# Kernel tuning notes

Hardware: AMD Instinct MI355X
Metric: run time of the kernel (lower is better)

Reference implementation:

```python
import jax, jax.numpy as jnp
import numpy as np

N, D_IN, D_OUT, K = 8192, 64, 128, 16


def setup_inputs() -> dict:
    key = jax.random.key(0)
    k1, k2, k3 = jax.random.split(key, 3)
    x = jax.random.normal(k1, (N, D_IN), dtype=jnp.float32)
    W1 = jax.random.normal(k2, (2 * D_IN, D_OUT), dtype=jnp.float32) * 0.05
    b1 = jnp.zeros((D_OUT,), dtype=jnp.float32)
    W2 = jax.random.normal(k3, (D_OUT, D_OUT), dtype=jnp.float32) * 0.05
    b2 = jnp.zeros((D_OUT,), dtype=jnp.float32)
    return {"x": x, "W1": W1, "b1": b1, "W2": W2, "b2": b2, "k": K}


def reference(x, W1, b1, W2, b2, k):
    # dynamic kNN graph (PyG knn(x, x, k) includes self as nearest neighbor)
    sq = jnp.sum(x * x, axis=-1)                      # [N]
    dist = sq[:, None] + sq[None, :] - 2.0 * (x @ x.T)  # [N, N] squared dists
    _, idx = jax.lax.top_k(-dist, k)                  # [N, k] nearest indices
    x_j = x[idx]                                      # [N, k, D_IN] gather
    x_i = jnp.broadcast_to(x[:, None, :], x_j.shape)  # [N, k, D_IN]
    e = jnp.concatenate([x_i, x_j - x_i], axis=-1)    # [N, k, 2*D_IN]
    h = jax.nn.relu(e @ W1 + b1) @ W2 + b2            # [N, k, D_OUT]
    return jnp.mean(h, axis=1)                        # mean aggregation -> [N, D_OUT]
```

## Files before the change

### kernel.cpp

```cpp
#include <hip/hip_runtime.h>

#define N 8192
#define DIN 64
#define DOUT 128
#define KNN 16
#define MSAMP 2048
#define NBX 8
#define CAND_R 64
#define CAND_C (NBX * CAND_R)
#define EPS 1.0f
#define DELTA_Q 64
#define VCAP 128
#define ROWS_PRE 16

typedef unsigned long long u64;
typedef __attribute__((ext_vector_type(8))) short bf16x8;
typedef __attribute__((ext_vector_type(4))) float floatx4;

__device__ __forceinline__ unsigned mono(float f) {
    unsigned u = __float_as_uint(f);
    return (u & 0x80000000u) ? ~u : (u | 0x80000000u);
}
__device__ __forceinline__ unsigned short f2bf(float f) {
    unsigned u = __float_as_uint(f);
    return (unsigned short)((u + 0x7FFFu + ((u >> 16) & 1u)) >> 16);
}
__device__ __forceinline__ unsigned qdist(float dist) {
    int q = (int)(dist * 128.0f) + 2;
    q = max(q, 0); return (unsigned)min(q, 65535);
}

__global__ __launch_bounds__(256) void k_pre(const float* __restrict__ x,
                                             const float* __restrict__ W1,
                                             const float* __restrict__ b1,
                                             float* __restrict__ sq,
                                             float* __restrict__ sqs,
                                             unsigned short* __restrict__ Xh,
                                             float* __restrict__ U,
                                             float* __restrict__ V) {
    __shared__ float xs[ROWS_PRE][DIN];
    int t = threadIdx.x;
    int r0 = blockIdx.x * ROWS_PRE;
    float4 xv = ((const float4*)x)[(size_t)r0 * (DIN / 4) + t];
    ((float4*)xs)[t] = xv;
    ushort4 h4;
    h4.x = f2bf(xv.x); h4.y = f2bf(xv.y);
    h4.z = f2bf(xv.z); h4.w = f2bf(xv.w);
    *(ushort4*)&Xh[r0 * DIN + t * 4] = h4;
    __syncthreads();
    if (t < ROWS_PRE) {
        const float4* xr = (const float4*)xs[t];
        float s0 = 0.f, s1 = 0.f, s2 = 0.f, s3 = 0.f;
#pragma unroll
        for (int q = 0; q < DIN / 4; ++q) {
            float4 a = xr[q];
            s0 = fmaf(a.x, a.x, s0); s1 = fmaf(a.y, a.y, s1);
            s2 = fmaf(a.z, a.z, s2); s3 = fmaf(a.w, a.w, s3);
        }
        float sv = (s0 + s1) + (s2 + s3);
        sq[r0 + t] = sv;
        if ((t & 3) == 0) sqs[(r0 + t) >> 2] = sv;
    }
    int o = t & 127, g = t >> 7;
    float aU[8], aV[8];
#pragma unroll
    for (int u = 0; u < 8; ++u) { aU[u] = 0.f; aV[u] = 0.f; }
    for (int kk = 0; kk < DIN; ++kk) {
        float whi = W1[kk * DOUT + o];
        float wlo = W1[(DIN + kk) * DOUT + o];
        float wd = whi - wlo;
#pragma unroll
        for (int u = 0; u < 8; ++u) {
            float xvv = xs[g * 8 + u][kk];
            aU[u] = fmaf(xvv, wd, aU[u]);
            aV[u] = fmaf(xvv, wlo, aV[u]);
        }
    }
    float bb = b1[o];
#pragma unroll
    for (int u = 0; u < 8; ++u) {
        int r = r0 + g * 8 + u;
        U[(size_t)r * DOUT + o] = aU[u] + bb;
        V[(size_t)r * DOUT + o] = aV[u];
    }
}

__global__ __launch_bounds__(512, 4) void k_pretau(const unsigned short* __restrict__ Xh,
                                                   const float* __restrict__ sq,
                                                   const float* __restrict__ sqs,
                                                   float* __restrict__ tauf) {
    __shared__ __align__(16) unsigned short qls[16 * MSAMP];
    int tid = threadIdx.x, w = tid >> 6, l = tid & 63;
    int m = l & 15, quad = l >> 4, ko = quad * 8;
    int rt = blockIdx.x;
    int irow = rt * 16 + m;
    size_t arow = (size_t)irow * DIN;
    bf16x8 iH0 = *(const bf16x8*)(Xh + arow + ko);
    bf16x8 iH1 = *(const bf16x8*)(Xh + arow + 32 + ko);
    float si = sq[irow];
    int swz = (m & 7) << 4;
    for (int it = 0; it < 16; ++it) {
        int s16 = w * 256 + it * 16;
        size_t srowA = (size_t)(4 * (s16 + m)) * DIN;
        bf16x8 sH0 = *(const bf16x8*)(Xh + srowA + ko);
        bf16x8 sH1 = *(const bf16x8*)(Xh + srowA + 32 + ko);
        floatx4 acc = {0.f, 0.f, 0.f, 0.f};
        acc = __builtin_amdgcn_mfma_f32_16x16x32_bf16(sH0, iH0, acc, 0, 0, 0);
        acc = __builtin_amdgcn_mfma_f32_16x16x32_bf16(sH1, iH1, acc, 0, 0, 0);
        int sc0 = s16 + quad * 4;
        float4 sj = *(const float4*)(sqs + sc0);
        unsigned q0 = qdist(fmaf(-2.0f, acc[0], si + sj.x));
        unsigned q1 = qdist(fmaf(-2.0f, acc[1], si + sj.y));
        unsigned q2 = qdist(fmaf(-2.0f, acc[2], si + sj.z));
        unsigned q3 = qdist(fmaf(-2.0f, acc[3], si + sj.w));
        u64 pk = (u64)q0 | ((u64)q1 << 16) | ((u64)q2 << 32) | ((u64)q3 << 48);
        *(u64*)&qls[m * MSAMP + (sc0 ^ swz)] = pk;
    }
    __syncthreads();
#pragma unroll
    for (int rr = 0; rr < 2; ++rr) {
        int rsub = w * 2 + rr;
        unsigned v[MSAMP / 64];
#pragma unroll
        for (int u = 0; u < MSAMP / 64; ++u)
            v[u] = qls[rsub * MSAMP + l + 64 * u];
        unsigned p = 0;
#pragma unroll
        for (int b = 15; b >= 0; --b) {
            unsigned c16 = p | (1u << b);
            int cnt = 0;
#pragma unroll
            for (int u = 0; u < MSAMP / 64; ++u)
                cnt += __popcll(__ballot(v[u] < c16));
            if (cnt < 16) p = c16;
        }
        if (l == 0) tauf[rt * 16 + rsub] = (float)p * (1.0f / 128.0f);
    }
}

__global__ __launch_bounds__(256, 4) void k_main(const unsigned short* __restrict__ Xh,
                                                 const float* __restrict__ sq,
                                                 const float* __restrict__ tauf,
                                                 unsigned* __restrict__ cand,
                                                 unsigned* __restrict__ cntpart) {
    __shared__ __align__(16) short ldsH[64 * 72];
    int tid = threadIdx.x, w = tid >> 6, l = tid & 63;
    int m = l & 15, ko = (l >> 4) * 8;
    int bx = blockIdx.x;
    int rt = blockIdx.y * 4 + w;
    size_t arow = (size_t)(rt * 16 + m) * DIN;
    bf16x8 aH0 = *(const bf16x8*)(Xh + arow + ko);
    bf16x8 aH1 = *(const bf16x8*)(Xh + arow + 32 + ko);
    int rg[4]; float T[4]; float si[4]; int rowcnt[4];
#pragma unroll
    for (int reg = 0; reg < 4; ++reg) {
        rg[reg] = rt * 16 + (l >> 4) * 4 + reg;
        si[reg] = sq[rg[reg]];
        T[reg] = tauf[rg[reg]] + EPS - si[reg];
        rowcnt[reg] = 0;
    }
    int qs = l & 48;
    unsigned lmask = (1u << (l & 15)) - 1u;
    int srw = tid >> 3, scol8 = (tid & 7) * 8;

    for (int st = 0; st < 16; ++st) {
        int jbase = bx * 1024 + st * 64;
        __syncthreads();
        *(bf16x8*)&ldsH[srw * 72 + scol8] =
            *(const bf16x8*)(Xh + (size_t)(jbase + srw) * DIN + scol8);
        *(bf16x8*)&ldsH[(srw + 32) * 72 + scol8] =
            *(const bf16x8*)(Xh + (size_t)(jbase + srw + 32) * DIN + scol8);
        __syncthreads();
#pragma unroll
        for (int it = 0; it < 4; ++it) {
            int br = it * 16 + m;
            bf16x8 bH0 = *(const bf16x8*)&ldsH[br * 72 + ko];
            bf16x8 bH1 = *(const bf16x8*)&ldsH[br * 72 + 32 + ko];
            floatx4 acc = {0.f, 0.f, 0.f, 0.f};
            acc = __builtin_amdgcn_mfma_f32_16x16x32_bf16(aH0, bH0, acc, 0, 0, 0);
            acc = __builtin_amdgcn_mfma_f32_16x16x32_bf16(aH1, bH1, acc, 0, 0, 0);
            int jcol = jbase + it * 16 + m;
            float sqj = sq[jcol];
#pragma unroll
            for (int reg = 0; reg < 4; ++reg) {
                float tv = fmaf(-2.0f, acc[reg], sqj);
                bool pass = tv <= T[reg];
                u64 bal = __ballot(pass);
                if (bal) {
                    unsigned m16 = (unsigned)((bal >> qs) & 0xFFFFull);
                    if (pass) {
                        int slot = rowcnt[reg] + __popc(m16 & lmask);
                        if (slot < CAND_R)
                            cand[(size_t)rg[reg] * CAND_C + bx * CAND_R + slot] =
                                (qdist(tv + si[reg]) << 16) | (unsigned)jcol;
                    }
                    rowcnt[reg] += __popc(m16);
                }
            }
        }
    }
    if ((l & 15) == 0) {
#pragma unroll
        for (int reg = 0; reg < 4; ++reg)
            cntpart[rg[reg] * NBX + bx] = (unsigned)min(rowcnt[reg], CAND_R);
    }
}

__global__ __launch_bounds__(256) void k_exact(const float* __restrict__ x,
                                               const float* __restrict__ sq,
                                               const unsigned* __restrict__ cntpart,
                                               const unsigned* __restrict__ cand,
                                               int* __restrict__ knn) {
    __shared__ unsigned cj[4][CAND_C];
    __shared__ unsigned short vlist[4][VCAP];
    __shared__ u64 ekeys[4][VCAP];
    int w = threadIdx.x >> 6, l = threadIdx.x & 63;
    int row = blockIdx.x * 4 + w;
    int base = 0;
#pragma unroll
    for (int b = 0; b < NBX; ++b) {
        int c = (int)cntpart[row * NBX + b];
        c = min(c, CAND_R);
        if (l < c) cj[w][base + l] = cand[(size_t)row * CAND_C + b * CAND_R + l];
        base += c;
    }
    __syncthreads();
    unsigned kk[CAND_C / 64], qq[CAND_C / 64];
#pragma unroll
    for (int u = 0; u < CAND_C / 64; ++u) {
        int idx = l + 64 * u;
        kk[u] = (idx < base) ? cj[w][idx] : 0xFFFFFFFFu;
        qq[u] = (idx < base) ? (kk[u] >> 16) : 0xFFFFFFFFu;
    }
    unsigned p = 0;
#pragma unroll
    for (int b = 15; b >= 0; --b) {
        unsigned c16 = p | (1u << b);
        int cnt = 0;
#pragma unroll
        for (int u = 0; u < CAND_C / 64; ++u)
            cnt += __popcll(__ballot(qq[u] < c16));
        if (cnt < 16) p = c16;
    }
    unsigned thr = p + DELTA_Q;
    int nv = 0;
    u64 lm = (l == 63) ? 0xFFFFFFFFFFFFFFFFull >> 1 : (1ull << l) - 1ull;
#pragma unroll
    for (int u = 0; u < CAND_C / 64; ++u) {
        bool pred = qq[u] <= thr;
        u64 bal = __ballot(pred);
        int slot = nv + __popcll(bal & lm);
        if (pred && slot < VCAP) vlist[w][slot] = (unsigned short)(kk[u] & 0xFFFFu);
        nv += __popcll(bal);
    }
    nv = min(nv, VCAP);
    __syncthreads();
    float sqi = sq[row];
    const float* xi = x + (size_t)row * DIN;
#pragma unroll
    for (int r = 0; r < VCAP / 64; ++r) {
        int v = l + 64 * r;
        if (v < nv) {
            int j = (int)vlist[w][v];
            const float4* bj = (const float4*)(x + (size_t)j * DIN);
            float4 rb[16];
#pragma unroll
            for (int q = 0; q < DIN / 4; ++q) rb[q] = bj[q];
            float s0 = 0.f, s1 = 0.f, s2 = 0.f, s3 = 0.f;
#pragma unroll
            for (int q = 0; q < DIN / 4; ++q) {
                s0 = fmaf(xi[4 * q + 0], rb[q].x, s0);
                s1 = fmaf(xi[4 * q + 1], rb[q].y, s1);
                s2 = fmaf(xi[4 * q + 2], rb[q].z, s2);
                s3 = fmaf(xi[4 * q + 3], rb[q].w, s3);
            }
            float d = (s0 + s1) + (s2 + s3);
            float dist = fmaf(-2.0f, d, sqi + sq[j]);
            ekeys[w][v] = ((u64)mono(dist) << 32) | (unsigned)j;
        }
    }
#pragma unroll
    for (int r = 0; r < VCAP / 64; ++r) {
        int v = l + 64 * r;
        if (v < nv) {
            u64 mykey = ekeys[w][v];
            int rank = 0;
            for (int i = 0; i < nv; ++i)
                rank += (ekeys[w][i] < mykey) ? 1 : 0;
            if (rank < KNN)
                knn[row * KNN + rank] = (int)(unsigned)(mykey & 0xFFFFFFFFull);
        }
    }
}

__global__ __launch_bounds__(256) void k_aggout(const float* __restrict__ U,
                                                const float* __restrict__ V,
                                                const int* __restrict__ knn,
                                                const float* __restrict__ W2,
                                                const float* __restrict__ b2,
                                                float* __restrict__ out) {
    __shared__ float ag[8][DOUT];
    __shared__ float w2t[32 * DOUT];
    int t = threadIdx.x;
    int o = t & 127, g = t >> 7;
    int i0 = blockIdx.x * 8 + g * 4;
#pragma unroll
    for (int r = 0; r < 4; ++r) {
        int i = i0 + r;
        float u = U[(size_t)i * DOUT + o];
        const int* nb = knn + i * KNN;
        float acc = 0.f;
#pragma unroll
        for (int q = 0; q < KNN; ++q)
            acc += fmaxf(u + V[(size_t)nb[q] * DOUT + o], 0.0f);
        ag[g * 4 + r][o] = acc * (1.0f / KNN);
    }
    float a2[4] = {0.f, 0.f, 0.f, 0.f};
#pragma unroll
    for (int tile = 0; tile < 4; ++tile) {
        __syncthreads();
#pragma unroll
        for (int u = 0; u < 4; ++u)
            ((float4*)w2t)[t + u * 256] =
                ((const float4*)(W2 + tile * 32 * DOUT))[t + u * 256];
        __syncthreads();
#pragma unroll 8
        for (int kk = 0; kk < 32; ++kk) {
            float wv = w2t[kk * DOUT + o];
#pragma unroll
            for (int r = 0; r < 4; ++r)
                a2[r] = fmaf(ag[g * 4 + r][tile * 32 + kk], wv, a2[r]);
        }
    }
    float bb = b2[o];
#pragma unroll
    for (int r = 0; r < 4; ++r)
        out[(size_t)(i0 + r) * DOUT + o] = a2[r] + bb;
}

extern "C" void kernel_launch(void* const* d_in, const int* in_sizes, int n_in,
                              void* d_out, int out_size, void* d_ws, size_t ws_size,
                              hipStream_t stream) {
    const float* x  = (const float*)d_in[0];
    const float* W1 = (const float*)d_in[1];
    const float* b1 = (const float*)d_in[2];
    const float* W2 = (const float*)d_in[3];
    const float* b2 = (const float*)d_in[4];
    float* out = (float*)d_out;

    char* ws = (char*)d_ws;
    float*          sq      = (float*)(ws);
    float*          sqs     = (float*)(ws + 32768);
    float*          tauf    = (float*)(ws + 40960);
    int*            knn     = (int*)(ws + 73728);
    unsigned short* Xh      = (unsigned short*)(ws + 655360);
    unsigned*       cntpart = (unsigned*)(ws + 1703936);
    float*          U       = (float*)(ws + 2097152);
    float*          V       = (float*)(ws + 6291456);
    unsigned*       cand    = (unsigned*)(ws + 10485760);

    k_pre<<<N / ROWS_PRE, 256, 0, stream>>>(x, W1, b1, sq, sqs, Xh, U, V);
    k_pretau<<<N / 16, 512, 0, stream>>>(Xh, sq, sqs, tauf);
    k_main<<<dim3(NBX, 128), 256, 0, stream>>>(Xh, sq, tauf, cand, cntpart);
    k_exact<<<N / 4, 256, 0, stream>>>(x, sq, cntpart, cand, knn);
    k_aggout<<<N / 8, 256, 0, stream>>>(U, V, knn, W2, b2, out);
}
```

Before: 182.0 us.

## Fuse pre, tau and candidate scan into one persistent kernel with grid barriers

Merges the preprocessing, threshold-estimation and candidate-scan kernels into a single 512-block persistent kernel that separates the phases with atomic grid barriers. It also merges exact kNN selection with aggregation and output, so the kNN indices stay in LDS instead of round-tripping through global memory. The aim is to cut kernel launch gaps and the tail effects between stages. In exchange it relies on all 512 blocks being co-resident for the spin barrier, and it changes the per-block work split (512 threads, one row-load per stage in the scan).

New measurement: 240.6 us. 32.2% more time.

```diff
diff --git a/kernel.cpp b/kernel.cpp
--- a/kernel.cpp
+++ b/kernel.cpp
@@ -11,7 +11,7 @@
 #define EPS 1.0f
 #define DELTA_Q 64
 #define VCAP 128
-#define ROWS_PRE 16
+#define NBLK 512
 
 typedef unsigned long long u64;
 typedef __attribute__((ext_vector_type(8))) short bf16x8;
@@ -30,312 +30,325 @@
     q = max(q, 0); return (unsigned)min(q, 65535);
 }
 
-__global__ __launch_bounds__(256) void k_pre(const float* __restrict__ x,
-                                             const float* __restrict__ W1,
-                                             const float* __restrict__ b1,
-                                             float* __restrict__ sq,
-                                             float* __restrict__ sqs,
-                                             unsigned short* __restrict__ Xh,
-                                             float* __restrict__ U,
-                                             float* __restrict__ V) {
-    __shared__ float xs[ROWS_PRE][DIN];
+__device__ __forceinline__ void gridbar(unsigned* cnt) {
+    __syncthreads();
+    if (threadIdx.x == 0) {
+        __hip_atomic_fetch_add(cnt, 1u, __ATOMIC_RELEASE, __HIP_MEMORY_SCOPE_AGENT);
+        while (__hip_atomic_load(cnt, __ATOMIC_RELAXED, __HIP_MEMORY_SCOPE_AGENT)
+               < (unsigned)NBLK)
+            __builtin_amdgcn_s_sleep(16);
+        __threadfence();
+    }
+    __syncthreads();
+}
+
+__global__ __launch_bounds__(512, 4) void k_scan(
+    const float* __restrict__ x, const float* __restrict__ W1,
+    const float* __restrict__ b1, float* __restrict__ sq,
+    float* __restrict__ sqs, unsigned short* __restrict__ Xh,
+    float* __restrict__ U, float* __restrict__ V,
+    float* __restrict__ tauf, unsigned* __restrict__ cand,
+    unsigned* __restrict__ cntpart, unsigned* __restrict__ bar)
+{
+    __shared__ __align__(16) unsigned char smem[65536];
     int t = threadIdx.x;
-    int r0 = blockIdx.x * ROWS_PRE;
-    float4 xv = ((const float4*)x)[(size_t)r0 * (DIN / 4) + t];
-    ((float4*)xs)[t] = xv;
-    ushort4 h4;
-    h4.x = f2bf(xv.x); h4.y = f2bf(xv.y);
-    h4.z = f2bf(xv.z); h4.w = f2bf(xv.w);
-    *(ushort4*)&Xh[r0 * DIN + t * 4] = h4;
-    __syncthreads();
-    if (t < ROWS_PRE) {
-        const float4* xr = (const float4*)xs[t];
-        float s0 = 0.f, s1 = 0.f, s2 = 0.f, s3 = 0.f;
-#pragma unroll
-        for (int q = 0; q < DIN / 4; ++q) {
-            float4 a = xr[q];
-            s0 = fmaf(a.x, a.x, s0); s1 = fmaf(a.y, a.y, s1);
-            s2 = fmaf(a.z, a.z, s2); s3 = fmaf(a.w, a.w, s3);
-        }
-        float sv = (s0 + s1) + (s2 + s3);
-        sq[r0 + t] = sv;
-        if ((t & 3) == 0) sqs[(r0 + t) >> 2] = sv;
-    }
-    int o = t & 127, g = t >> 7;
-    float aU[8], aV[8];
-#pragma unroll
-    for (int u = 0; u < 8; ++u) { aU[u] = 0.f; aV[u] = 0.f; }
-    for (int kk = 0; kk < DIN; ++kk) {
-        float whi = W1[kk * DOUT + o];
-        float wlo = W1[(DIN + kk) * DOUT + o];
-        float wd = whi - wlo;
-#pragma unroll
-        for (int u = 0; u < 8; ++u) {
-            float xvv = xs[g * 8 + u][kk];
-            aU[u] = fmaf(xvv, wd, aU[u]);
-            aV[u] = fmaf(xvv, wlo, aV[u]);
-        }
-    }
-    float bb = b1[o];
-#pragma unroll
-    for (int u = 0; u < 8; ++u) {
-        int r = r0 + g * 8 + u;
-        U[(size_t)r * DOUT + o] = aU[u] + bb;
-        V[(size_t)r * DOUT + o] = aV[u];
-    }
-}
-
-__global__ __launch_bounds__(512, 4) void k_pretau(const unsigned short* __restrict__ Xh,
-                                                   const float* __restrict__ sq,
-                                                   const float* __restrict__ sqs,
-                                                   float* __restrict__ tauf) {
-    __shared__ __align__(16) unsigned short qls[16 * MSAMP];
-    int tid = threadIdx.x, w = tid >> 6, l = tid & 63;
-    int m = l & 15, quad = l >> 4, ko = quad * 8;
-    int rt = blockIdx.x;
-    int irow = rt * 16 + m;
-    size_t arow = (size_t)irow * DIN;
-    bf16x8 iH0 = *(const bf16x8*)(Xh + arow + ko);
-    bf16x8 iH1 = *(const bf16x8*)(Xh + arow + 32 + ko);
-    float si = sq[irow];
-    int swz = (m & 7) << 4;
-    for (int it = 0; it < 16; ++it) {
-        int s16 = w * 256 + it * 16;
-        size_t srowA = (size_t)(4 * (s16 + m)) * DIN;
-        bf16x8 sH0 = *(const bf16x8*)(Xh + srowA + ko);
-        bf16x8 sH1 = *(const bf16x8*)(Xh + srowA + 32 + ko);
-        floatx4 acc = {0.f, 0.f, 0.f, 0.f};
-        acc = __builtin_amdgcn_mfma_f32_16x16x32_bf16(sH0, iH0, acc, 0, 0, 0);
-        acc = __builtin_amdgcn_mfma_f32_16x16x32_bf16(sH1, iH1, acc, 0, 0, 0);
-        int sc0 = s16 + quad * 4;
-        float4 sj = *(const float4*)(sqs + sc0);
-        unsigned q0 = qdist(fmaf(-2.0f, acc[0], si + sj.x));
-        unsigned q1 = qdist(fmaf(-2.0f, acc[1], si + sj.y));
-        unsigned q2 = qdist(fmaf(-2.0f, acc[2], si + sj.z));
-        unsigned q3 = qdist(fmaf(-2.0f, acc[3], si + sj.w));
-        u64 pk = (u64)q0 | ((u64)q1 << 16) | ((u64)q2 << 32) | ((u64)q3 << 48);
-        *(u64*)&qls[m * MSAMP + (sc0 ^ swz)] = pk;
-    }
-    __syncthreads();
-#pragma unroll
-    for (int rr = 0; rr < 2; ++rr) {
-        int rsub = w * 2 + rr;
-        unsigned v[MSAMP / 64];
-#pragma unroll
-        for (int u = 0; u < MSAMP / 64; ++u)
-            v[u] = qls[rsub * MSAMP + l + 64 * u];
+    int b = blockIdx.x;
+
+    {
+        float (*xs)[DIN] = (float (*)[DIN])smem;
+        int r0 = b * 16;
+        if (t < 256) {
+            float4 xv = ((const float4*)x)[(size_t)r0 * (DIN / 4) + t];
+            ((float4*)xs)[t] = xv;
+            ushort4 h4;
+            h4.x = f2bf(xv.x); h4.y = f2bf(xv.y);
+            h4.z = f2bf(xv.z); h4.w = f2bf(xv.w);
+            *(ushort4*)&Xh[r0 * DIN + t * 4] = h4;
+        }
+        __syncthreads();
+        if (t < 16) {
+            const float4* xr = (const float4*)xs[t];
+            float s0 = 0.f, s1 = 0.f, s2 = 0.f, s3 = 0.f;
+#pragma unroll
+            for (int q = 0; q < DIN / 4; ++q) {
+                float4 a = xr[q];
+                s0 = fmaf(a.x, a.x, s0); s1 = fmaf(a.y, a.y, s1);
+                s2 = fmaf(a.z, a.z, s2); s3 = fmaf(a.w, a.w, s3);
+            }
+            float sv = (s0 + s1) + (s2 + s3);
+            sq[r0 + t] = sv;
+            if ((t & 3) == 0) sqs[(r0 + t) >> 2] = sv;
+        }
+        int o = t & 127, g = t >> 7;
+        float aU[4], aV[4];
+#pragma unroll
+        for (int u = 0; u < 4; ++u) { aU[u] = 0.f; aV[u] = 0.f; }
+        for (int kk = 0; kk < DIN; ++kk) {
+            float whi = W1[kk * DOUT + o];
+            float wlo = W1[(DIN + kk) * DOUT + o];
+            float wd = whi - wlo;
+#pragma unroll
+            for (int u = 0; u < 4; ++u) {
+                float xvv = xs[g * 4 + u][kk];
+                aU[u] = fmaf(xvv, wd, aU[u]);
+                aV[u] = fmaf(xvv, wlo, aV[u]);
+            }
+        }
+        float bb = b1[o];
+#pragma unroll
+        for (int u = 0; u < 4; ++u) {
+            int r = r0 + g * 4 + u;
+            U[(size_t)r * DOUT + o] = aU[u] + bb;
+            V[(size_t)r * DOUT + o] = aV[u];
+        }
+    }
+    gridbar(bar);
+    {
+        unsigned short* qls = (unsigned short*)smem;
+        int w = t >> 6, l = t & 63;
+        int m = l & 15, quad = l >> 4, ko = quad * 8;
+        int irow = b * 16 + m;
+        size_t arow = (size_t)irow * DIN;
+        bf16x8 iH0 = *(const bf16x8*)(Xh + arow + ko);
+        bf16x8 iH1 = *(const bf16x8*)(Xh + arow + 32 + ko);
+        float si = sq[irow];
+        int swz = (m & 7) << 4;
+        for (int it = 0; it < 16; ++it) {
+            int s16 = w * 256 + it * 16;
+            size_t srowA = (size_t)(4 * (s16 + m)) * DIN;
+            bf16x8 sH0 = *(const bf16x8*)(Xh + srowA + ko);
+            bf16x8 sH1 = *(const bf16x8*)(Xh + srowA + 32 + ko);
+            floatx4 acc = {0.f, 0.f, 0.f, 0.f};
+            acc = __builtin_amdgcn_mfma_f32_16x16x32_bf16(sH0, iH0, acc, 0, 0, 0);
+            acc = __builtin_amdgcn_mfma_f32_16x16x32_bf16(sH1, iH1, acc, 0, 0, 0);
+            int sc0 = s16 + quad * 4;
+            float4 sj = *(const float4*)(sqs + sc0);
+            unsigned q0 = qdist(fmaf(-2.0f, acc[0], si + sj.x));
+            unsigned q1 = qdist(fmaf(-2.0f, acc[1], si + sj.y));
+            unsigned q2 = qdist(fmaf(-2.0f, acc[2], si + sj.z));
+            unsigned q3 = qdist(fmaf(-2.0f, acc[3], si + sj.w));
+            u64 pk = (u64)q0 | ((u64)q1 << 16) | ((u64)q2 << 32) | ((u64)q3 << 48);
+            *(u64*)&qls[m * MSAMP + (sc0 ^ swz)] = pk;
+        }
+        __syncthreads();
+#pragma unroll
+        for (int rr = 0; rr < 2; ++rr) {
+            int rsub = w * 2 + rr;
+            unsigned v[MSAMP / 64];
+#pragma unroll
+            for (int u = 0; u < MSAMP / 64; ++u)
+                v[u] = qls[rsub * MSAMP + l + 64 * u];
+            unsigned p = 0;
+#pragma unroll
+            for (int bb = 15; bb >= 0; --bb) {
+                unsigned c16 = p | (1u << bb);
+                int cnt = 0;
+#pragma unroll
+                for (int u = 0; u < MSAMP / 64; ++u)
+                    cnt += __popcll(__ballot(v[u] < c16));
+                if (cnt < 16) p = c16;
+            }
+            if (l == 0) tauf[b * 16 + rsub] = (float)p * (1.0f / 128.0f);
+        }
+    }
+    gridbar(bar + 1);
+    {
+        short* ldsH = (short*)smem;
+        int w = t >> 6, l = t & 63;
+        int m = l & 15, ko = (l >> 4) * 8;
+        int bx = b & 7;
+        int rt = (b >> 3) * 8 + w;
+        size_t arow = (size_t)(rt * 16 + m) * DIN;
+        bf16x8 aH0 = *(const bf16x8*)(Xh + arow + ko);
+        bf16x8 aH1 = *(const bf16x8*)(Xh + arow + 32 + ko);
+        int rg[4]; float T[4]; float si[4]; int rowcnt[4];
+#pragma unroll
+        for (int reg = 0; reg < 4; ++reg) {
+            rg[reg] = rt * 16 + (l >> 4) * 4 + reg;
+            si[reg] = sq[rg[reg]];
+            T[reg] = tauf[rg[reg]] + EPS - si[reg];
+            rowcnt[reg] = 0;
+        }
+        int qs = l & 48;
+        unsigned lmask = (1u << (l & 15)) - 1u;
+        int srw = t >> 3, scol8 = (t & 7) * 8;
+
+        for (int st = 0; st < 16; ++st) {
+            int jbase = bx * 1024 + st * 64;
+            __syncthreads();
+            *(bf16x8*)&ldsH[srw * 72 + scol8] =
+                *(const bf16x8*)(Xh + (size_t)(jbase + srw) * DIN + scol8);
+            __syncthreads();
+#pragma unroll
+            for (int it = 0; it < 4; ++it) {
+                int br = it * 16 + m;
+                bf16x8 bH0 = *(const bf16x8*)&ldsH[br * 72 + ko];
+                bf16x8 bH1 = *(const bf16x8*)&ldsH[br * 72 + 32 + ko];
+                floatx4 acc = {0.f, 0.f, 0.f, 0.f};
+                acc = __builtin_amdgcn_mfma_f32_16x16x32_bf16(aH0, bH0, acc, 0, 0, 0);
+                acc = __builtin_amdgcn_mfma_f32_16x16x32_bf16(aH1, bH1, acc, 0, 0, 0);
+                int jcol = jbase + it * 16 + m;
+                float sqj = sq[jcol];
+#pragma unroll
+                for (int reg = 0; reg < 4; ++reg) {
+                    float tv = fmaf(-2.0f, acc[reg], sqj);
+                    bool pass = tv <= T[reg];
+                    u64 bal = __ballot(pass);
+                    if (bal) {
+                        unsigned m16 = (unsigned)((bal >> qs) & 0xFFFFull);
+                        if (pass) {
+                            int slot = rowcnt[reg] + __popc(m16 & lmask);
+                            if (slot < CAND_R)
+                                cand[(size_t)rg[reg] * CAND_C + bx * CAND_R + slot] =
+                                    (qdist(tv + si[reg]) << 16) | (unsigned)jcol;
+                        }
+                        rowcnt[reg] += __popc(m16);
+                    }
+                }
+            }
+        }
+        if ((l & 15) == 0) {
+#pragma unroll
+            for (int reg = 0; reg < 4; ++reg)
+                cntpart[rg[reg] * NBX + bx] = (unsigned)min(rowcnt[reg], CAND_R);
+        }
+    }
+}
+
+__global__ __launch_bounds__(256) void k_post(
+    const float* __restrict__ x, const float* __restrict__ sq,
+    const unsigned* __restrict__ cntpart, const unsigned* __restrict__ cand,
+    const float* __restrict__ U, const float* __restrict__ V,
+    const float* __restrict__ W2, const float* __restrict__ b2,
+    float* __restrict__ out)
+{
+    __shared__ union {
+        struct { unsigned cj[4][CAND_C];
+                 unsigned short vlist[4][VCAP];
+                 u64 ekeys[4][VCAP]; } e;
+        struct { float ag[4][DOUT];
+                 float w2t[32 * DOUT]; } a;
+    } sm;
+    __shared__ int knn_s[4][KNN];
+    int t = threadIdx.x;
+    int w = t >> 6, l = t & 63;
+    int row = blockIdx.x * 4 + w;
+    {
+        int base = 0;
+#pragma unroll
+        for (int b = 0; b < NBX; ++b) {
+            int c = (int)cntpart[row * NBX + b];
+            c = min(c, CAND_R);
+            if (l < c) sm.e.cj[w][base + l] =
+                cand[(size_t)row * CAND_C + b * CAND_R + l];
+            base += c;
+        }
+        __syncthreads();
+        unsigned kk[CAND_C / 64], qq[CAND_C / 64];
+#pragma unroll
+        for (int u = 0; u < CAND_C / 64; ++u) {
+            int idx = l + 64 * u;
+            kk[u] = (idx < base) ? sm.e.cj[w][idx] : 0xFFFFFFFFu;
+            qq[u] = (idx < base) ? (kk[u] >> 16) : 0xFFFFFFFFu;
+        }
         unsigned p = 0;
 #pragma unroll
         for (int b = 15; b >= 0; --b) {
             unsigned c16 = p | (1u << b);
             int cnt = 0;
 #pragma unroll
-            for (int u = 0; u < MSAMP / 64; ++u)
-                cnt += __popcll(__ballot(v[u] < c16));
+            for (int u = 0; u < CAND_C / 64; ++u)
+                cnt += __popcll(__ballot(qq[u] < c16));
             if (cnt < 16) p = c16;
         }
-        if (l == 0) tauf[rt * 16 + rsub] = (float)p * (1.0f / 128.0f);
-    }
-}
-
-__global__ __launch_bounds__(256, 4) void k_main(const unsigned short* __restrict__ Xh,
-                                                 const float* __restrict__ sq,
-                                                 const float* __restrict__ tauf,
-                                                 unsigned* __restrict__ cand,
-                                                 unsigned* __restrict__ cntpart) {
-    __shared__ __align__(16) short ldsH[64 * 72];
-    int tid = threadIdx.x, w = tid >> 6, l = tid & 63;
-    int m = l & 15, ko = (l >> 4) * 8;
-    int bx = blockIdx.x;
-    int rt = blockIdx.y * 4 + w;
-    size_t arow = (size_t)(rt * 16 + m) * DIN;
-    bf16x8 aH0 = *(const bf16x8*)(Xh + arow + ko);
-    bf16x8 aH1 = *(const bf16x8*)(Xh + arow + 32 + ko);
-    int rg[4]; float T[4]; float si[4]; int rowcnt[4];
-#pragma unroll
-    for (int reg = 0; reg < 4; ++reg) {
-        rg[reg] = rt * 16 + (l >> 4) * 4 + reg;
-        si[reg] = sq[rg[reg]];
-        T[reg] = tauf[rg[reg]] + EPS - si[reg];
-        rowcnt[reg] = 0;
-    }
-    int qs = l & 48;
-    unsigned lmask = (1u << (l & 15)) - 1u;
-    int srw = tid >> 3, scol8 = (tid & 7) * 8;
-
-    for (int st = 0; st < 16; ++st) {
-        int jbase = bx * 1024 + st * 64;
+        unsigned thr = p + DELTA_Q;
+        int nv = 0;
+        u64 lm = (l == 63) ? 0xFFFFFFFFFFFFFFFFull >> 1 : (1ull << l) - 1ull;
+#pragma unroll
+        for (int u = 0; u < CAND_C / 64; ++u) {
+            bool pred = qq[u] <= thr;
+            u64 bal = __ballot(pred);
+            int slot = nv + __popcll(bal & lm);
+            if (pred && slot < VCAP)
+                sm.e.vlist[w][slot] = (unsigned short)(kk[u] & 0xFFFFu);
+            nv += __popcll(bal);
+        }
+        nv = min(nv, VCAP);
         __syncthreads();
-        *(bf16x8*)&ldsH[srw * 72 + scol8] =
-            *(const bf16x8*)(Xh + (size_t)(jbase + srw) * DIN + scol8);
-        *(bf16x8*)&ldsH[(srw + 32) * 72 + scol8] =
-            *(const bf16x8*)(Xh + (size_t)(jbase + srw + 32) * DIN + scol8);
-        __syncthreads();
-#pragma unroll
-        for (int it = 0; it < 4; ++it) {
-            int br = it * 16 + m;
-            bf16x8 bH0 = *(const bf16x8*)&ldsH[br * 72 + ko];
-            bf16x8 bH1 = *(const bf16x8*)&ldsH[br * 72 + 32 + ko];
-            floatx4 acc = {0.f, 0.f, 0.f, 0.f};
-            acc = __builtin_amdgcn_mfma_f32_16x16x32_bf16(aH0, bH0, acc, 0, 0, 0);
-            acc = __builtin_amdgcn_mfma_f32_16x16x32_bf16(aH1, bH1, acc, 0, 0, 0);
-            int jcol = jbase + it * 16 + m;
-            float sqj = sq[jcol];
-#pragma unroll
-            for (int reg = 0; reg < 4; ++reg) {
-                float tv = fmaf(-2.0f, acc[reg], sqj);
-                bool pass = tv <= T[reg];
-                u64 bal = __ballot(pass);
-                if (bal) {
-                    unsigned m16 = (unsigned)((bal >> qs) & 0xFFFFull);
-                    if (pass) {
-                        int slot = rowcnt[reg] + __popc(m16 & lmask);
-                        if (slot < CAND_R)
-                            cand[(size_t)rg[reg] * CAND_C + bx * CAND_R + slot] =
-                                (qdist(tv + si[reg]) << 16) | (unsigned)jcol;
-                    }
-                    rowcnt[reg] += __popc(m16);
+        float sqi = sq[row];
+        const float* xi = x + (size_t)row * DIN;
+#pragma unroll
+        for (int r = 0; r < VCAP / 64; ++r) {
+            int v = l + 64 * r;
+            if (v < nv) {
+                int j = (int)sm.e.vlist[w][v];
+                const float4* bj = (const float4*)(x + (size_t)j * DIN);
+                float4 rb[16];
+#pragma unroll
+                for (int q = 0; q < DIN / 4; ++q) rb[q] = bj[q];
+                float s0 = 0.f, s1 = 0.f, s2 = 0.f, s3 = 0.f;
+#pragma unroll
+                for (int q = 0; q < DIN / 4; ++q) {
+                    s0 = fmaf(xi[4 * q + 0], rb[q].x, s0);
+                    s1 = fmaf(xi[4 * q + 1], rb[q].y, s1);
+                    s2 = fmaf(xi[4 * q + 2], rb[q].z, s2);
+                    s3 = fmaf(xi[4 * q + 3], rb[q].w, s3);
                 }
-            }
-        }
-    }
-    if ((l & 15) == 0) {
-#pragma unroll
-        for (int reg = 0; reg < 4; ++reg)
-            cntpart[rg[reg] * NBX + bx] = (unsigned)min(rowcnt[reg], CAND_R);
-    }
-}
-
-__global__ __launch_bounds__(256) void k_exact(const float* __restrict__ x,
-                                               const float* __restrict__ sq,
-                                               const unsigned* __restrict__ cntpart,
-                                               const unsigned* __restrict__ cand,
-                                               int* __restrict__ knn) {
-    __shared__ unsigned cj[4][CAND_C];
-    __shared__ unsigned short vlist[4][VCAP];
-    __shared__ u64 ekeys[4][VCAP];
-    int w = threadIdx.x >> 6, l = threadIdx.x & 63;
-    int row = blockIdx.x * 4 + w;
-    int base = 0;
-#pragma unroll
-    for (int b = 0; b < NBX; ++b) {
-        int c = (int)cntpart[row * NBX + b];
-        c = min(c, CAND_R);
-        if (l < c) cj[w][base + l] = cand[(size_t)row * CAND_C + b * CAND_R + l];
-        base += c;
+                float d = (s0 + s1) + (s2 + s3);
+                float dist = fmaf(-2.0f, d, sqi + sq[j]);
+                sm.e.ekeys[w][v] = ((u64)mono(dist) << 32) | (unsigned)j;
+            }
+        }
+#pragma unroll
+        for (int r = 0; r < VCAP / 64; ++r) {
+            int v = l + 64 * r;
+            if (v < nv) {
+                u64 mykey = sm.e.ekeys[w][v];
+                int rank = 0;
+                for (int i = 0; i < nv; ++i)
+                    rank += (sm.e.ekeys[w][i] < mykey) ? 1 : 0;
+                if (rank < KNN)
+                    knn_s[w][rank] = (int)(unsigned)(mykey & 0xFFFFFFFFull);
+            }
+        }
     }
     __syncthreads();
-    unsigned kk[CAND_C / 64], qq[CAND_C / 64];
-#pragma unroll
-    for (int u = 0; u < CAND_C / 64; ++u) {
-        int idx = l + 64 * u;
-        kk[u] = (idx < base) ? cj[w][idx] : 0xFFFFFFFFu;
-        qq[u] = (idx < base) ? (kk[u] >> 16) : 0xFFFFFFFFu;
-    }
-    unsigned p = 0;
-#pragma unroll
-    for (int b = 15; b >= 0; --b) {
-        unsigned c16 = p | (1u << b);
-        int cnt = 0;
-#pragma unroll
-        for (int u = 0; u < CAND_C / 64; ++u)
-            cnt += __popcll(__ballot(qq[u] < c16));
-        if (cnt < 16) p = c16;
-    }
-    unsigned thr = p + DELTA_Q;
-    int nv = 0;
-    u64 lm = (l == 63) ? 0xFFFFFFFFFFFFFFFFull >> 1 : (1ull << l) - 1ull;
-#pragma unroll
-    for (int u = 0; u < CAND_C / 64; ++u) {
-        bool pred = qq[u] <= thr;
-        u64 bal = __ballot(pred);
-        int slot = nv + __popcll(bal & lm);
-        if (pred && slot < VCAP) vlist[w][slot] = (unsigned short)(kk[u] & 0xFFFFu);
-        nv += __popcll(bal);
-    }
-    nv = min(nv, VCAP);
-    __syncthreads();
-    float sqi = sq[row];
-    const float* xi = x + (size_t)row * DIN;
-#pragma unroll
-    for (int r = 0; r < VCAP / 64; ++r) {
-        int v = l + 64 * r;
-        if (v < nv) {
-            int j = (int)vlist[w][v];
-            const float4* bj = (const float4*)(x + (size_t)j * DIN);
-            float4 rb[16];
-#pragma unroll
-            for (int q = 0; q < DIN / 4; ++q) rb[q] = bj[q];
-            float s0 = 0.f, s1 = 0.f, s2 = 0.f, s3 = 0.f;
-#pragma unroll
-            for (int q = 0; q < DIN / 4; ++q) {
-                s0 = fmaf(xi[4 * q + 0], rb[q].x, s0);
-                s1 = fmaf(xi[4 * q + 1], rb[q].y, s1);
-                s2 = fmaf(xi[4 * q + 2], rb[q].z, s2);
-                s3 = fmaf(xi[4 * q + 3], rb[q].w, s3);
-            }
-            float d = (s0 + s1) + (s2 + s3);
-            float dist = fmaf(-2.0f, d, sqi + sq[j]);
-            ekeys[w][v] = ((u64)mono(dist) << 32) | (unsigned)j;
-        }
-    }
-#pragma unroll
-    for (int r = 0; r < VCAP / 64; ++r) {
-        int v = l + 64 * r;
-        if (v < nv) {
-            u64 mykey = ekeys[w][v];
-            int rank = 0;
-            for (int i = 0; i < nv; ++i)
-                rank += (ekeys[w][i] < mykey) ? 1 : 0;
-            if (rank < KNN)
-                knn[row * KNN + rank] = (int)(unsigned)(mykey & 0xFFFFFFFFull);
-        }
-    }
-}
-
-__global__ __launch_bounds__(256) void k_aggout(const float* __restrict__ U,
-                                                const float* __restrict__ V,
-                                                const int* __restrict__ knn,
-                                                const float* __restrict__ W2,
-                                                const float* __restrict__ b2,
-                                                float* __restrict__ out) {
-    __shared__ float ag[8][DOUT];
-    __shared__ float w2t[32 * DOUT];
-    int t = threadIdx.x;
-    int o = t & 127, g = t >> 7;
-    int i0 = blockIdx.x * 8 + g * 4;
-#pragma unroll
-    for (int r = 0; r < 4; ++r) {
-        int i = i0 + r;
-        float u = U[(size_t)i * DOUT + o];
-        const int* nb = knn + i * KNN;
-        float acc = 0.f;
-#pragma unroll
-        for (int q = 0; q < KNN; ++q)
-            acc += fmaxf(u + V[(size_t)nb[q] * DOUT + o], 0.0f);
-        ag[g * 4 + r][o] = acc * (1.0f / KNN);
-    }
-    float a2[4] = {0.f, 0.f, 0.f, 0.f};
-#pragma unroll
-    for (int tile = 0; tile < 4; ++tile) {
-        __syncthreads();
-#pragma unroll
-        for (int u = 0; u < 4; ++u)
-            ((float4*)w2t)[t + u * 256] =
-                ((const float4*)(W2 + tile * 32 * DOUT))[t + u * 256];
-        __syncthreads();
+    {
+        int o = t & 127, g = t >> 7;
+        int row0 = blockIdx.x * 4;
+#pragma unroll
+        for (int r = 0; r < 2; ++r) {
+            int rr = g * 2 + r;
+            int i = row0 + rr;
+            float u = U[(size_t)i * DOUT + o];
+            float acc = 0.f;
+#pragma unroll
+            for (int q = 0; q < KNN; ++q)
+                acc += fmaxf(u + V[(size_t)knn_s[rr][q] * DOUT + o], 0.0f);
+            sm.a.ag[rr][o] = acc * (1.0f / KNN);
+        }
+        float a2[2] = {0.f, 0.f};
+#pragma unroll
+        for (int tile = 0; tile < 4; ++tile) {
+            __syncthreads();
+#pragma unroll
+            for (int u = 0; u < 4; ++u)
+                ((float4*)sm.a.w2t)[t + u * 256] =
+                    ((const float4*)(W2 + tile * 32 * DOUT))[t + u * 256];
+            __syncthreads();
 #pragma unroll 8
-        for (int kk = 0; kk < 32; ++kk) {
-            float wv = w2t[kk * DOUT + o];
-#pragma unroll
-            for (int r = 0; r < 4; ++r)
-                a2[r] = fmaf(ag[g * 4 + r][tile * 32 + kk], wv, a2[r]);
-        }
-    }
-    float bb = b2[o];
-#pragma unroll
-    for (int r = 0; r < 4; ++r)
-        out[(size_t)(i0 + r) * DOUT + o] = a2[r] + bb;
+            for (int kk = 0; kk < 32; ++kk) {
+                float wv = sm.a.w2t[kk * DOUT + o];
+#pragma unroll
+                for (int r = 0; r < 2; ++r)
+                    a2[r] = fmaf(sm.a.ag[g * 2 + r][tile * 32 + kk], wv, a2[r]);
+            }
+        }
+        float bb = b2[o];
+#pragma unroll
+        for (int r = 0; r < 2; ++r)
+            out[(size_t)(row0 + g * 2 + r) * DOUT + o] = a2[r] + bb;
+    }
 }
 
 extern "C" void kernel_launch(void* const* d_in, const int* in_sizes, int n_in,
@@ -352,16 +365,15 @@
     float*          sq      = (float*)(ws);
     float*          sqs     = (float*)(ws + 32768);
     float*          tauf    = (float*)(ws + 40960);
-    int*            knn     = (int*)(ws + 73728);
+    unsigned*       bar     = (unsigned*)(ws + 73728);
     unsigned short* Xh      = (unsigned short*)(ws + 655360);
     unsigned*       cntpart = (unsigned*)(ws + 1703936);
     float*          U       = (float*)(ws + 2097152);
     float*          V       = (float*)(ws + 6291456);
     unsigned*       cand    = (unsigned*)(ws + 10485760);
 
-    k_pre<<<N / ROWS_PRE, 256, 0, stream>>>(x, W1, b1, sq, sqs, Xh, U, V);
-    k_pretau<<<N / 16, 512, 0, stream>>>(Xh, sq, sqs, tauf);
-    k_main<<<dim3(NBX, 128), 256, 0, stream>>>(Xh, sq, tauf, cand, cntpart);
-    k_exact<<<N / 4, 256, 0, stream>>>(x, sq, cntpart, cand, knn);
-    k_aggout<<<N / 8, 256, 0, stream>>>(U, V, knn, W2, b2, out);
-}
+    hipMemsetAsync(bar, 0, 8, stream);
+    k_scan<<<NBLK, 512, 0, stream>>>(x, W1, b1, sq, sqs, Xh, U, V,
+                                     tauf, cand, cntpart, bar);
+    k_post<<<N / 4, 256, 0, stream>>>(x, sq, cntpart, cand, U, V, W2, b2, out);
+}
```

## Fuse exact kNN refinement with aggregation and double candidate-scan split

Applied to the files above, without the earlier changes.

Merges the exact-distance refinement kernel and the aggregation/output kernel into one kernel. The kNN indices now stay in shared memory, and the two stages share LDS through a union. This removes one launch and the global round trip for the kNN indices. The candidate scan also gets twice as many column blocks (16 instead of 8), each with half as many tiles and a higher occupancy hint. That gives more parallelism, but doubles the candidate buffer and the number of per-block candidate lists each row must merge. The fused kernel computes only 2 output rows per thread group instead of 4, so W2 is reloaded into LDS twice as often per row.

Measured after the change: 185.5 us. About the same (+1.9%).

```diff
diff --git a/kernel.cpp b/kernel.cpp
--- a/kernel.cpp
+++ b/kernel.cpp
@@ -5,7 +5,8 @@
 #define DOUT 128
 #define KNN 16
 #define MSAMP 2048
-#define NBX 8
+#define NBX 16
+#define NST 8
 #define CAND_R 64
 #define CAND_C (NBX * CAND_R)
 #define EPS 1.0f
@@ -138,7 +139,7 @@
     }
 }
 
-__global__ __launch_bounds__(256, 4) void k_main(const unsigned short* __restrict__ Xh,
+__global__ __launch_bounds__(256, 8) void k_main(const unsigned short* __restrict__ Xh,
                                                  const float* __restrict__ sq,
                                                  const float* __restrict__ tauf,
                                                  unsigned* __restrict__ cand,
@@ -163,8 +164,8 @@
     unsigned lmask = (1u << (l & 15)) - 1u;
     int srw = tid >> 3, scol8 = (tid & 7) * 8;
 
-    for (int st = 0; st < 16; ++st) {
-        int jbase = bx * 1024 + st * 64;
+    for (int st = 0; st < NST; ++st) {
+        int jbase = bx * (NST * 64) + st * 64;
         __syncthreads();
         *(bf16x8*)&ldsH[srw * 72 + scol8] =
             *(const bf16x8*)(Xh + (size_t)(jbase + srw) * DIN + scol8);
@@ -206,136 +207,140 @@
     }
 }
 
-__global__ __launch_bounds__(256) void k_exact(const float* __restrict__ x,
-                                               const float* __restrict__ sq,
-                                               const unsigned* __restrict__ cntpart,
-                                               const unsigned* __restrict__ cand,
-                                               int* __restrict__ knn) {
-    __shared__ unsigned cj[4][CAND_C];
-    __shared__ unsigned short vlist[4][VCAP];
-    __shared__ u64 ekeys[4][VCAP];
-    int w = threadIdx.x >> 6, l = threadIdx.x & 63;
+__global__ __launch_bounds__(256) void k_post(
+    const float* __restrict__ x, const float* __restrict__ sq,
+    const unsigned* __restrict__ cntpart, const unsigned* __restrict__ cand,
+    const float* __restrict__ U, const float* __restrict__ V,
+    const float* __restrict__ W2, const float* __restrict__ b2,
+    float* __restrict__ out)
+{
+    __shared__ union {
+        struct { unsigned cj[4][CAND_C];
+                 unsigned short vlist[4][VCAP];
+                 u64 ekeys[4][VCAP]; } e;
+        struct { float ag[4][DOUT];
+                 float w2t[32 * DOUT]; } a;
+    } sm;
+    __shared__ int knn_s[4][KNN];
+    int t = threadIdx.x;
+    int w = t >> 6, l = t & 63;
     int row = blockIdx.x * 4 + w;
-    int base = 0;
-#pragma unroll
-    for (int b = 0; b < NBX; ++b) {
-        int c = (int)cntpart[row * NBX + b];
-        c = min(c, CAND_R);
-        if (l < c) cj[w][base + l] = cand[(size_t)row * CAND_C + b * CAND_R + l];
-        base += c;
+    {
+        int base = 0;
+#pragma unroll
+        for (int b = 0; b < NBX; ++b) {
+            int c = (int)cntpart[row * NBX + b];
+            c = min(c, CAND_R);
+            if (l < c) sm.e.cj[w][base + l] =
+                cand[(size_t)row * CAND_C + b * CAND_R + l];
+            base += c;
+        }
+        __syncthreads();
+        unsigned kk[CAND_C / 64], qq[CAND_C / 64];
+#pragma unroll
+        for (int u = 0; u < CAND_C / 64; ++u) {
+            int idx = l + 64 * u;
+            kk[u] = (idx < base) ? sm.e.cj[w][idx] : 0xFFFFFFFFu;
+            qq[u] = (idx < base) ? (kk[u] >> 16) : 0xFFFFFFFFu;
+        }
+        unsigned p = 0;
+#pragma unroll
+        for (int b = 15; b >= 0; --b) {
+            unsigned c16 = p | (1u << b);
+            int cnt = 0;
+#pragma unroll
+            for (int u = 0; u < CAND_C / 64; ++u)
+                cnt += __popcll(__ballot(qq[u] < c16));
+            if (cnt < 16) p = c16;
+        }
+        unsigned thr = p + DELTA_Q;
+        int nv = 0;
+        u64 lm = (l == 63) ? 0xFFFFFFFFFFFFFFFFull >> 1 : (1ull << l) - 1ull;
+#pragma unroll
+        for (int u = 0; u < CAND_C / 64; ++u) {
+            bool pred = qq[u] <= thr;
+            u64 bal = __ballot(pred);
+            int slot = nv + __popcll(bal & lm);
+            if (pred && slot < VCAP)
+                sm.e.vlist[w][slot] = (unsigned short)(kk[u] & 0xFFFFu);
+            nv += __popcll(bal);
+        }
+        nv = min(nv, VCAP);
+        __syncthreads();
+        float sqi = sq[row];
+        const float* xi = x + (size_t)row * DIN;
+#pragma unroll
+        for (int r = 0; r < VCAP / 64; ++r) {
+            int v = l + 64 * r;
+            if (v < nv) {
+                int j = (int)sm.e.vlist[w][v];
+                const float4* bj = (const float4*)(x + (size_t)j * DIN);
+                float4 rb[16];
+#pragma unroll
+                for (int q = 0; q < DIN / 4; ++q) rb[q] = bj[q];
+                float s0 = 0.f, s1 = 0.f, s2 = 0.f, s3 = 0.f;
+#pragma unroll
+                for (int q = 0; q < DIN / 4; ++q) {
+                    s0 = fmaf(xi[4 * q + 0], rb[q].x, s0);
+                    s1 = fmaf(xi[4 * q + 1], rb[q].y, s1);
+                    s2 = fmaf(xi[4 * q + 2], rb[q].z, s2);
+                    s3 = fmaf(xi[4 * q + 3], rb[q].w, s3);
+                }
+                float d = (s0 + s1) + (s2 + s3);
+                float dist = fmaf(-2.0f, d, sqi + sq[j]);
+                sm.e.ekeys[w][v] = ((u64)mono(dist) << 32) | (unsigned)j;
+            }
+        }
+#pragma unroll
+        for (int r = 0; r < VCAP / 64; ++r) {
+            int v = l + 64 * r;
+            if (v < nv) {
+                u64 mykey = sm.e.ekeys[w][v];
+                int rank = 0;
+                for (int i = 0; i < nv; ++i)
+                    rank += (sm.e.ekeys[w][i] < mykey) ? 1 : 0;
+                if (rank < KNN)
+                    knn_s[w][rank] = (int)(unsigned)(mykey & 0xFFFFFFFFull);
+            }
+        }
     }
     __syncthreads();
-    unsigned kk[CAND_C / 64], qq[CAND_C / 64];
-#pragma unroll
-    for (int u = 0; u < CAND_C / 64; ++u) {
-        int idx = l + 64 * u;
-        kk[u] = (idx < base) ? cj[w][idx] : 0xFFFFFFFFu;
-        qq[u] = (idx < base) ? (kk[u] >> 16) : 0xFFFFFFFFu;
-    }
-    unsigned p = 0;
-#pragma unroll
-    for (int b = 15; b >= 0; --b) {
-        unsigned c16 = p | (1u << b);
-        int cnt = 0;
-#pragma unroll
-        for (int u = 0; u < CAND_C / 64; ++u)
-            cnt += __popcll(__ballot(qq[u] < c16));
-        if (cnt < 16) p = c16;
-    }
-    unsigned thr = p + DELTA_Q;
-    int nv = 0;
-    u64 lm = (l == 63) ? 0xFFFFFFFFFFFFFFFFull >> 1 : (1ull << l) - 1ull;
-#pragma unroll
-    for (int u = 0; u < CAND_C / 64; ++u) {
-        bool pred = qq[u] <= thr;
-        u64 bal = __ballot(pred);
-        int slot = nv + __popcll(bal & lm);
-        if (pred && slot < VCAP) vlist[w][slot] = (unsigned short)(kk[u] & 0xFFFFu);
-        nv += __popcll(bal);
-    }
-    nv = min(nv, VCAP);
-    __syncthreads();
-    float sqi = sq[row];
-    const float* xi = x + (size_t)row * DIN;
-#pragma unroll
-    for (int r = 0; r < VCAP / 64; ++r) {
-        int v = l + 64 * r;
-        if (v < nv) {
-            int j = (int)vlist[w][v];
-            const float4* bj = (const float4*)(x + (size_t)j * DIN);
-            float4 rb[16];
-#pragma unroll
-            for (int q = 0; q < DIN / 4; ++q) rb[q] = bj[q];
-            float s0 = 0.f, s1 = 0.f, s2 = 0.f, s3 = 0.f;
-#pragma unroll
-            for (int q = 0; q < DIN / 4; ++q) {
-                s0 = fmaf(xi[4 * q + 0], rb[q].x, s0);
-                s1 = fmaf(xi[4 * q + 1], rb[q].y, s1);
-                s2 = fmaf(xi[4 * q + 2], rb[q].z, s2);
-                s3 = fmaf(xi[4 * q + 3], rb[q].w, s3);
+    {
+        int o = t & 127, g = t >> 7;
+        int row0 = blockIdx.x * 4;
+#pragma unroll
+        for (int r = 0; r < 2; ++r) {
+            int rr = g * 2 + r;
+            int i = row0 + rr;
+            float u = U[(size_t)i * DOUT + o];
+            float acc = 0.f;
+#pragma unroll
+            for (int q = 0; q < KNN; ++q)
+                acc += fmaxf(u + V[(size_t)knn_s[rr][q] * DOUT + o], 0.0f);
+            sm.a.ag[rr][o] = acc * (1.0f / KNN);
+        }
+        float a2[2] = {0.f, 0.f};
+#pragma unroll
+        for (int tile = 0; tile < 4; ++tile) {
+            __syncthreads();
+#pragma unroll
+            for (int u = 0; u < 4; ++u)
+                ((float4*)sm.a.w2t)[t + u * 256] =
+                    ((const float4*)(W2 + tile * 32 * DOUT))[t + u * 256];
+            __syncthreads();
+#pragma unroll 8
+            for (int kk = 0; kk < 32; ++kk) {
+                float wv = sm.a.w2t[kk * DOUT + o];
+#pragma unroll
+                for (int r = 0; r < 2; ++r)
+                    a2[r] = fmaf(sm.a.ag[g * 2 + r][tile * 32 + kk], wv, a2[r]);
             }
-            float d = (s0 + s1) + (s2 + s3);
-            float dist = fmaf(-2.0f, d, sqi + sq[j]);
-            ekeys[w][v] = ((u64)mono(dist) << 32) | (unsigned)j;
-        }
-    }
-#pragma unroll
-    for (int r = 0; r < VCAP / 64; ++r) {
-        int v = l + 64 * r;
-        if (v < nv) {
-            u64 mykey = ekeys[w][v];
-            int rank = 0;
-            for (int i = 0; i < nv; ++i)
-                rank += (ekeys[w][i] < mykey) ? 1 : 0;
-            if (rank < KNN)
-                knn[row * KNN + rank] = (int)(unsigned)(mykey & 0xFFFFFFFFull);
-        }
-    }
-}
-
-__global__ __launch_bounds__(256) void k_aggout(const float* __restrict__ U,
-                                                const float* __restrict__ V,
-                                                const int* __restrict__ knn,
-                                                const float* __restrict__ W2,
-                                                const float* __restrict__ b2,
-                                                float* __restrict__ out) {
-    __shared__ float ag[8][DOUT];
-    __shared__ float w2t[32 * DOUT];
-    int t = threadIdx.x;
-    int o = t & 127, g = t >> 7;
-    int i0 = blockIdx.x * 8 + g * 4;
-#pragma unroll
-    for (int r = 0; r < 4; ++r) {
-        int i = i0 + r;
-        float u = U[(size_t)i * DOUT + o];
-        const int* nb = knn + i * KNN;
-        float acc = 0.f;
-#pragma unroll
-        for (int q = 0; q < KNN; ++q)
-            acc += fmaxf(u + V[(size_t)nb[q] * DOUT + o], 0.0f);
-        ag[g * 4 + r][o] = acc * (1.0f / KNN);
-    }
-    float a2[4] = {0.f, 0.f, 0.f, 0.f};
-#pragma unroll
-    for (int tile = 0; tile < 4; ++tile) {
-        __syncthreads();
-#pragma unroll
-        for (int u = 0; u < 4; ++u)
-            ((float4*)w2t)[t + u * 256] =
-                ((const float4*)(W2 + tile * 32 * DOUT))[t + u * 256];
-        __syncthreads();
-#pragma unroll 8
-        for (int kk = 0; kk < 32; ++kk) {
-            float wv = w2t[kk * DOUT + o];
-#pragma unroll
-            for (int r = 0; r < 4; ++r)
-                a2[r] = fmaf(ag[g * 4 + r][tile * 32 + kk], wv, a2[r]);
-        }
-    }
-    float bb = b2[o];
-#pragma unroll
-    for (int r = 0; r < 4; ++r)
-        out[(size_t)(i0 + r) * DOUT + o] = a2[r] + bb;
+        }
+        float bb = b2[o];
+#pragma unroll
+        for (int r = 0; r < 2; ++r)
+            out[(size_t)(row0 + g * 2 + r) * DOUT + o] = a2[r] + bb;
+    }
 }
 
 extern "C" void kernel_launch(void* const* d_in, const int* in_sizes, int n_in,
@@ -352,16 +357,14 @@
     float*          sq      = (float*)(ws);
     float*          sqs     = (float*)(ws + 32768);
     float*          tauf    = (float*)(ws + 40960);
-    int*            knn     = (int*)(ws + 73728);
     unsigned short* Xh      = (unsigned short*)(ws + 655360);
-    unsigned*       cntpart = (unsigned*)(ws + 1703936);
     float*          U       = (float*)(ws + 2097152);
     float*          V       = (float*)(ws + 6291456);
-    unsigned*       cand    = (unsigned*)(ws + 10485760);
+    unsigned*       cntpart = (unsigned*)(ws + 10485760);
+    unsigned*       cand    = (unsigned*)(ws + 11534336);
 
     k_pre<<<N / ROWS_PRE, 256, 0, stream>>>(x, W1, b1, sq, sqs, Xh, U, V);
     k_pretau<<<N / 16, 512, 0, stream>>>(Xh, sq, sqs, tauf);
     k_main<<<dim3(NBX, 128), 256, 0, stream>>>(Xh, sq, tauf, cand, cntpart);
-    k_exact<<<N / 4, 256, 0, stream>>>(x, sq, cntpart, cand, knn);
-    k_aggout<<<N / 8, 256, 0, stream>>>(U, V, knn, W2, b2, out);
-}
+    k_post<<<N / 4, 256, 0, stream>>>(x, sq, cntpart, cand, U, V, W2, b2, out);
+}
```
